# Optimization experiments

Hardware: AMD Instinct MI355X
Metric: run time of the kernel (lower is better)

Reference implementation:

```python
import jax, jax.numpy as jnp
import numpy as np

N_VERTICES = 1_000_000
N_EDGES = 32_000_000


def setup_inputs() -> dict:
    key = jax.random.key(0)
    k1, k2, k3 = jax.random.split(key, 3)
    vertex_attr = jax.random.normal(k1, (N_VERTICES, 2), dtype=jnp.float32)
    edgeij_pair = jax.random.randint(k2, (2, N_EDGES), 0, N_VERTICES, dtype=jnp.int64)
    edge_attr = jax.random.normal(k3, (N_EDGES, 1), dtype=jnp.float32)
    g = jnp.zeros((1, 1), dtype=jnp.float32)
    batch = jnp.zeros((N_VERTICES,), dtype=jnp.int64)
    return {"vertex_attr": vertex_attr, "edgeij_pair": edgeij_pair,
            "edge_attr": edge_attr, "g": g, "batch": batch}


def reference(vertex_attr, edgeij_pair, edge_attr, g, batch):
    # b_i = first feature column of each vertex, kept as [N, 1]
    b_i = vertex_attr[:, 0:1]
    n_vertices = b_i.shape[0]
    # edge_aggregation_function: scatter-sum edge attrs onto destination vertex
    dst = edgeij_pair[1]  # [E]
    cbar_i = jax.ops.segment_sum(edge_attr, dst, num_segments=n_vertices)  # [N, 1]
    y_i = b_i * cbar_i
    return jnp.concatenate([b_i, y_i], axis=1)  # [N, 2]
```

## Files before the change

### kernel.cpp

```cpp
#include <hip/hip_runtime.h>


#define VB_SHIFT 13
#define VB       (1 << VB_SHIFT)
#define NBUCKETS 128
#define TPB      512
#define TILE     8192
#define RSLICES  8
#define RTPB     512
#define FXSCALE  8192.0f
#define FXINV    (1.0f / 8192.0f)

typedef int   iv4 __attribute__((ext_vector_type(4)));
typedef float fv4 __attribute__((ext_vector_type(4)));
typedef unsigned uv4 __attribute__((ext_vector_type(4)));

__device__ __forceinline__ unsigned pack_edge(int d, float v) {
    int fx = __float2int_rn(v * FXSCALE);
    fx = max(-(1 << 18) + 1, min((1 << 18) - 1, fx));
    return ((unsigned)fx << VB_SHIFT) | (unsigned)(d & (VB - 1));
}

__global__ void __launch_bounds__(TPB)
sort_tiles(const int* __restrict__ dst,
           const float* __restrict__ val,
           int* __restrict__ starts_t,
           unsigned* __restrict__ pairs,
           int n_e, int ntp) {
    __shared__ int cnt[NBUCKETS];
    __shared__ int loff[NBUCKETS];
    __shared__ int wsum_s;
    __shared__ unsigned sorted[TILE];

    const int t = threadIdx.x;
    const int tile = blockIdx.x;
    const int base = tile * TILE;
    const int tn = min(TILE, n_e - base);

    if (t < NBUCKETS) cnt[t] = 0;
    __syncthreads();

    iv4 d[4]; fv4 v[4]; int rk[4][4]; int nval[4];
    if (tn == TILE) {
        #pragma unroll
        for (int q = 0; q < 4; ++q) {
            const int e0 = (q * TPB + t) * 4;
            d[q] = __builtin_nontemporal_load((const iv4*)(dst + base + e0));
            v[q] = __builtin_nontemporal_load((const fv4*)(val + base + e0));
            nval[q] = 4;
        }
        #pragma unroll
        for (int q = 0; q < 4; ++q) {
            rk[q][0] = atomicAdd(&cnt[d[q].x >> VB_SHIFT], 1);
            rk[q][1] = atomicAdd(&cnt[d[q].y >> VB_SHIFT], 1);
            rk[q][2] = atomicAdd(&cnt[d[q].z >> VB_SHIFT], 1);
            rk[q][3] = atomicAdd(&cnt[d[q].w >> VB_SHIFT], 1);
        }
    } else {
        #pragma unroll
        for (int q = 0; q < 4; ++q) {
            const int e0 = (q * TPB + t) * 4;
            nval[q] = max(0, min(4, tn - e0));
            #pragma unroll
            for (int k = 0; k < 4; ++k) {
                bool ok = k < nval[q];
                d[q][k] = ok ? dst[base + e0 + k] : 0;
                v[q][k] = ok ? val[base + e0 + k] : 0.f;
                rk[q][k] = ok ? atomicAdd(&cnt[d[q][k] >> VB_SHIFT], 1) : 0;
            }
        }
    }
    __syncthreads();

    int x = 0, incl = 0;
    if (t < NBUCKETS) {
        x = cnt[t];
        incl = x;
        #pragma unroll
        for (int off = 1; off < 64; off <<= 1) {
            int y = __shfl_up(incl, off, 64);
            if ((t & 63) >= off) incl += y;
        }
        if (t == 63) wsum_s = incl;
    }
    __syncthreads();
    if (t < NBUCKETS) {
        int e = incl - x + ((t >= 64) ? wsum_s : 0);
        loff[t] = e;
        starts_t[(size_t)t * ntp + tile] = base + e;
    }
    if (t == 0) starts_t[(size_t)NBUCKETS * ntp + tile] = base + tn;
    __syncthreads();

    #pragma unroll
    for (int q = 0; q < 4; ++q) {
        #pragma unroll
        for (int k = 0; k < 4; ++k) {
            if (k < nval[q]) {
                int b = d[q][k] >> VB_SHIFT;
                sorted[loff[b] + rk[q][k]] = pack_edge(d[q][k], v[q][k]);
            }
        }
    }
    __syncthreads();

    uv4* __restrict__ po = (uv4*)(pairs + base);
    const uv4* __restrict__ so = (const uv4*)sorted;
    #pragma unroll
    for (int q = 0; q < 4; ++q) {
        int i4 = q * TPB + t;
        if (i4 * 4 + 4 <= tn)      po[i4] = so[i4];
        else
            for (int i = i4 * 4; i < min(i4 * 4 + 4, tn); ++i)
                pairs[base + i] = sorted[i];
    }
}

#define LDSADD(P) atomicAdd(&acc[(P) & (VB - 1)], ((int)(P)) >> VB_SHIFT)

__global__ void __launch_bounds__(RTPB)
tile_reduce(const unsigned* __restrict__ pairs,
            const int* __restrict__ starts_t,
            int* __restrict__ partial,
            int ntiles, int ntp) {
    __shared__ int acc[VB];
    const int b = blockIdx.x >> 3;
    const int s = blockIdx.x & (RSLICES - 1);
    const int t = threadIdx.x;
    for (int i = t; i < (VB >> 2); i += RTPB) ((iv4*)acc)[i] = (iv4){0, 0, 0, 0};
    __syncthreads();

    const int per = (ntiles + RSLICES - 1) / RSLICES;
    const int lo = min(s * per, ntiles);
    const int hi = min(lo + per, ntiles);
    const int w = t >> 6, lane = t & 63;
    const int* __restrict__ srow = starts_t + (size_t)b * ntp;
    const int* __restrict__ erow = starts_t + (size_t)(b + 1) * ntp;

    for (int tb = lo + w * 64; tb < hi; tb += 8 * 64) {
        const int nc = min(64, hi - tb);
        int sv = (lane < nc) ? srow[tb + lane] : 0;
        int ev = (lane < nc) ? erow[tb + lane] : 0;
        for (int r = 0; r < nc; r += 2) {
            int s0a = __shfl(sv, r),     s1a = __shfl(ev, r);
            int s0b = 0, s1b = 0;
            if (r + 1 < nc) { s0b = __shfl(sv, r + 1); s1b = __shfl(ev, r + 1); }
            int ja = s0a + lane, jb = s0b + lane;
            while (ja < s1a || jb < s1b) {
                unsigned pa = (ja < s1a) ? pairs[ja] : 0u;
                unsigned pb = (jb < s1b) ? pairs[jb] : 0u;
                LDSADD(pa);
                LDSADD(pb);
                ja += 64; jb += 64;
            }
        }
    }
    __syncthreads();
    int* pp = partial + ((size_t)b * RSLICES + s) * VB;
    for (int i = t; i < (VB >> 2); i += RTPB)
        ((iv4*)pp)[i] = ((const iv4*)acc)[i];
}

__global__ void __launch_bounds__(TPB)
combine_out(const int* __restrict__ partial, const float* __restrict__ va,
            float* __restrict__ out, int n_v) {
    const int tid = blockIdx.x * blockDim.x + threadIdx.x;
    const int stride = gridDim.x * blockDim.x;
    const int n_q = n_v >> 2;
    for (int q = tid; q < n_q; q += stride) {
        int v = q << 2;
        int b = v >> VB_SHIFT;
        int idx = v & (VB - 1);
        const int* pb = partial + (size_t)b * RSLICES * VB + idx;
        iv4 ci = (iv4){0, 0, 0, 0};
        #pragma unroll
        for (int s = 0; s < RSLICES; ++s)
            ci += *(const iv4*)(pb + (size_t)s * VB);
        fv4 c = (fv4){ci.x * FXINV, ci.y * FXINV, ci.z * FXINV, ci.w * FXINV};
        fv4 a0 = ((const fv4*)va)[2 * q];
        fv4 a1 = ((const fv4*)va)[2 * q + 1];
        fv4 o0 = (fv4){a0.x, a0.x * c.x, a0.z, a0.z * c.y};
        fv4 o1 = (fv4){a1.x, a1.x * c.z, a1.z, a1.z * c.w};
        ((fv4*)out)[2 * q]     = o0;
        ((fv4*)out)[2 * q + 1] = o1;
    }
    for (int v = (n_q << 2) + tid; v < n_v; v += stride) {
        int b = v >> VB_SHIFT;
        int idx = v & (VB - 1);
        int ci = 0;
        for (int s = 0; s < RSLICES; ++s)
            ci += partial[((size_t)b * RSLICES + s) * VB + idx];
        float bb = va[2 * v];
        out[2 * v] = bb;
        out[2 * v + 1] = bb * (ci * FXINV);
    }
}

__global__ void scatter_add_dev(const int* __restrict__ dst,
                                const float* __restrict__ w,
                                float* __restrict__ cbar, int n_e) {
    const int tid = blockIdx.x * blockDim.x + threadIdx.x;
    const int stride = gridDim.x * blockDim.x;
    for (int j = tid; j < n_e; j += stride)
        atomicAdd(&cbar[dst[j]], w[j]);
}

__global__ void zero_f32(float* __restrict__ p, int n) {
    int i = blockIdx.x * blockDim.x + threadIdx.x;
    int stride = gridDim.x * blockDim.x;
    for (; i < n; i += stride) p[i] = 0.0f;
}

__global__ void finalize_single(const float* __restrict__ va,
                                const float* __restrict__ cbar,
                                float* __restrict__ out, int n_v) {
    const int tid = blockIdx.x * blockDim.x + threadIdx.x;
    const int stride = gridDim.x * blockDim.x;
    for (int i = tid; i < n_v; i += stride) {
        float bb = va[2 * i];
        float2 o; o.x = bb; o.y = bb * cbar[i];
        ((float2*)out)[i] = o;
    }
}

extern "C" void kernel_launch(void* const* d_in, const int* in_sizes, int n_in,
                              void* d_out, int out_size, void* d_ws, size_t ws_size,
                              hipStream_t stream) {
    const float* vertex_attr = (const float*)d_in[0];
    const int*   edgeij      = (const int*)d_in[1];
    const float* edge_attr   = (const float*)d_in[2];

    const int n_vertices = in_sizes[0] / 2;
    const int n_edges    = in_sizes[2];
    const int* dst = edgeij + n_edges;

    const int ntiles = (n_edges + TILE - 1) / TILE;
    const int ntp = (ntiles + 63) & ~63;

    char* base = (char*)d_ws;
    size_t off = 0;
    int* starts_t = (int*)(base + off);
    off += (size_t)(NBUCKETS + 1) * ntp * 4;
    off = (off + 255) & ~(size_t)255;
    const size_t partial_elems = (size_t)NBUCKETS * RSLICES * VB;
    int* partial = (int*)(base + off);
    off += partial_elems * 4;
    off = (off + 255) & ~(size_t)255;
    unsigned* pairs = (unsigned*)(base + off);
    const size_t pairs_bytes = (size_t)ntiles * TILE * 4;

    const bool aligned16 = (((uintptr_t)dst & 15) == 0) &&
                           (((uintptr_t)edge_attr & 15) == 0) &&
                           (((uintptr_t)pairs & 15) == 0);
    const bool fits = (n_vertices <= NBUCKETS * VB) &&
                      (ws_size >= off + pairs_bytes) && aligned16 && (ntiles > 0);

    if (fits) {
        sort_tiles <<<ntiles, TPB, 0, stream>>>(dst, edge_attr, starts_t,
                                                pairs, n_edges, ntp);
        tile_reduce<<<NBUCKETS * RSLICES, RTPB, 0, stream>>>(pairs, starts_t,
                                                             partial, ntiles, ntp);
        combine_out<<<512, TPB, 0, stream>>>(partial, vertex_attr,
                                             (float*)d_out, n_vertices);
    } else {
        float* cbar = (float*)d_ws;
        zero_f32<<<2048, 256, 0, stream>>>(cbar, n_vertices);
        int threads = 256;
        int blocks = (n_edges + threads - 1) / threads;
        if (blocks > 4096) blocks = 4096;
        scatter_add_dev<<<blocks, threads, 0, stream>>>(dst, edge_attr, cbar, n_edges);
        int fblocks = (n_vertices + threads - 1) / threads;
        if (fblocks > 2048) fblocks = 2048;
        finalize_single<<<fblocks, threads, 0, stream>>>(vertex_attr, cbar,
                                                         (float*)d_out, n_vertices);
    }
}
```

Measured before the change: 114.0 us.

## Fuse combine pass into tile_reduce via last-block-done ticket per bucket

Drops the separate combine_out launch. Each tile_reduce block takes a ticket from a per-bucket atomic counter after writing its partial histogram, and the last of the RSLICES blocks for that bucket sums the slices and writes the output. The counters are zeroed by tile 0 of sort_tiles. Block-to-(bucket, slice) mapping is also swapped so the slices of one bucket are spread across the grid. This removes one kernel launch and its tail, at the cost of threadfences and a serialized final pass done by only one block per bucket.

After: 354.3 us. 211% more time.

```diff
diff --git a/kernel.cpp b/kernel.cpp
--- a/kernel.cpp
+++ b/kernel.cpp
@@ -26,6 +26,7 @@
            const float* __restrict__ val,
            int* __restrict__ starts_t,
            unsigned* __restrict__ pairs,
+           int* __restrict__ counters,
            int n_e, int ntp) {
     __shared__ int cnt[NBUCKETS];
     __shared__ int loff[NBUCKETS];
@@ -36,6 +37,8 @@
     const int tile = blockIdx.x;
     const int base = tile * TILE;
     const int tn = min(TILE, n_e - base);
+
+    if (tile == 0 && t < NBUCKETS) counters[t] = 0;
 
     if (t < NBUCKETS) cnt[t] = 0;
     __syncthreads();
@@ -122,10 +125,13 @@
 tile_reduce(const unsigned* __restrict__ pairs,
             const int* __restrict__ starts_t,
             int* __restrict__ partial,
-            int ntiles, int ntp) {
+            int* __restrict__ counters,
+            const float* __restrict__ va,
+            float* __restrict__ out,
+            int ntiles, int ntp, int n_v) {
     __shared__ int acc[VB];
-    const int b = blockIdx.x >> 3;
-    const int s = blockIdx.x & (RSLICES - 1);
+    const int b = blockIdx.x & (NBUCKETS - 1);
+    const int s = blockIdx.x >> 7;
     const int t = threadIdx.x;
     for (int i = t; i < (VB >> 2); i += RTPB) ((iv4*)acc)[i] = (iv4){0, 0, 0, 0};
     __syncthreads();
@@ -159,37 +165,38 @@
     int* pp = partial + ((size_t)b * RSLICES + s) * VB;
     for (int i = t; i < (VB >> 2); i += RTPB)
         ((iv4*)pp)[i] = ((const iv4*)acc)[i];
-}
-
-__global__ void __launch_bounds__(TPB)
-combine_out(const int* __restrict__ partial, const float* __restrict__ va,
-            float* __restrict__ out, int n_v) {
-    const int tid = blockIdx.x * blockDim.x + threadIdx.x;
-    const int stride = gridDim.x * blockDim.x;
-    const int n_q = n_v >> 2;
-    for (int q = tid; q < n_q; q += stride) {
-        int v = q << 2;
-        int b = v >> VB_SHIFT;
-        int idx = v & (VB - 1);
-        const int* pb = partial + (size_t)b * RSLICES * VB + idx;
+
+    __threadfence();
+    __shared__ int ticket_s;
+    if (t == 0) ticket_s = atomicAdd(&counters[b], 1);
+    __syncthreads();
+    if (ticket_s != RSLICES - 1) return;
+    __threadfence();
+
+    const int vbase = b << VB_SHIFT;
+    const int vend = min(vbase + VB, n_v);
+    const int nv = vend - vbase;
+    if (nv <= 0) return;
+    const int nq = nv >> 2;
+    const int* __restrict__ pball = partial + (size_t)b * RSLICES * VB;
+    const size_t qbase = (size_t)(vbase >> 2);
+    for (int qi = t; qi < nq; qi += RTPB) {
         iv4 ci = (iv4){0, 0, 0, 0};
         #pragma unroll
-        for (int s = 0; s < RSLICES; ++s)
-            ci += *(const iv4*)(pb + (size_t)s * VB);
+        for (int s2 = 0; s2 < RSLICES; ++s2)
+            ci += *(const iv4*)(pball + (size_t)s2 * VB + qi * 4);
         fv4 c = (fv4){ci.x * FXINV, ci.y * FXINV, ci.z * FXINV, ci.w * FXINV};
-        fv4 a0 = ((const fv4*)va)[2 * q];
-        fv4 a1 = ((const fv4*)va)[2 * q + 1];
+        fv4 a0 = ((const fv4*)va)[(qbase + qi) * 2];
+        fv4 a1 = ((const fv4*)va)[(qbase + qi) * 2 + 1];
         fv4 o0 = (fv4){a0.x, a0.x * c.x, a0.z, a0.z * c.y};
         fv4 o1 = (fv4){a1.x, a1.x * c.z, a1.z, a1.z * c.w};
-        ((fv4*)out)[2 * q]     = o0;
-        ((fv4*)out)[2 * q + 1] = o1;
-    }
-    for (int v = (n_q << 2) + tid; v < n_v; v += stride) {
-        int b = v >> VB_SHIFT;
-        int idx = v & (VB - 1);
+        ((fv4*)out)[(qbase + qi) * 2]     = o0;
+        ((fv4*)out)[(qbase + qi) * 2 + 1] = o1;
+    }
+    for (int v = vbase + (nq << 2) + t; v < vend; v += RTPB) {
         int ci = 0;
-        for (int s = 0; s < RSLICES; ++s)
-            ci += partial[((size_t)b * RSLICES + s) * VB + idx];
+        for (int s2 = 0; s2 < RSLICES; ++s2)
+            ci += pball[(size_t)s2 * VB + (v - vbase)];
         float bb = va[2 * v];
         out[2 * v] = bb;
         out[2 * v + 1] = bb * (ci * FXINV);
@@ -241,6 +248,8 @@
     size_t off = 0;
     int* starts_t = (int*)(base + off);
     off += (size_t)(NBUCKETS + 1) * ntp * 4;
+    int* counters = (int*)(base + off);
+    off += (size_t)NBUCKETS * 4;
     off = (off + 255) & ~(size_t)255;
     const size_t partial_elems = (size_t)NBUCKETS * RSLICES * VB;
     int* partial = (int*)(base + off);
@@ -257,11 +266,13 @@
 
     if (fits) {
         sort_tiles <<<ntiles, TPB, 0, stream>>>(dst, edge_attr, starts_t,
-                                                pairs, n_edges, ntp);
+                                                pairs, counters, n_edges, ntp);
         tile_reduce<<<NBUCKETS * RSLICES, RTPB, 0, stream>>>(pairs, starts_t,
-                                                             partial, ntiles, ntp);
-        combine_out<<<512, TPB, 0, stream>>>(partial, vertex_attr,
-                                             (float*)d_out, n_vertices);
+                                                             partial, counters,
+                                                             vertex_attr,
+                                                             (float*)d_out,
+                                                             ntiles, ntp,
+                                                             n_vertices);
     } else {
         float* cbar = (float*)d_ws;
         zero_f32<<<2048, 256, 0, stream>>>(cbar, n_vertices);
```
